# Kernel tuning notes

Measured on AMD Instinct MI355X. Metric: run time of the kernel, lower is better.

Reference implementation:

```python
import jax, jax.numpy as jnp
import numpy as np

N_NODES = 50000


def gcn_conv(x, W, b, src, dst, n):
    """PyG GCNConv: add self-loops, sym-normalize, linear, scatter-add."""
    loop = jnp.arange(n, dtype=src.dtype)
    s = jnp.concatenate([src, loop])  # [E+N]
    d = jnp.concatenate([dst, loop])
    deg = jax.ops.segment_sum(jnp.ones_like(s, dtype=x.dtype), d, num_segments=n)
    dinv = jnp.where(deg > 0, jax.lax.rsqrt(deg), 0.0)  # deg^-1/2
    norm = dinv[s] * dinv[d]  # [E+N]
    h = x @ W  # [N, out] dense GEMM first (in >= out)
    msg = h[s] * norm[:, None]  # gather + scale
    out = jax.ops.segment_sum(msg, d, num_segments=n)  # scatter-add
    return out + b


def setup_inputs() -> dict:
    key = jax.random.key(0)
    k1, k2, k3, k4, k5, k6, k7, k8 = jax.random.split(key, 8)
    in_c, hid_c, out_c = 512, 128, 64
    n, e, l = N_NODES, 800000, 100000
    x = jax.random.normal(k1, (n, in_c), dtype=jnp.float32)
    edge_index = jax.random.randint(k2, (2, e), 0, n, dtype=jnp.int64)
    edge_label_index = jax.random.randint(k3, (2, l), 0, n, dtype=jnp.int64)
    # Glorot-ish init for weights, zeros for biases (PyG default bias=zeros)
    W1 = jax.random.normal(k4, (in_c, hid_c), dtype=jnp.float32) / np.sqrt(in_c)
    b1 = jnp.zeros((hid_c,), dtype=jnp.float32)
    W2 = jax.random.normal(k5, (hid_c, out_c), dtype=jnp.float32) / np.sqrt(hid_c)
    b2 = jnp.zeros((out_c,), dtype=jnp.float32)
    return {"x": x, "edge_index": edge_index, "edge_label_index": edge_label_index,
            "W1": W1, "b1": b1, "W2": W2, "b2": b2}


def reference(x, edge_index, edge_label_index, W1, b1, W2, b2):
    n = x.shape[0]
    src, dst = edge_index[0], edge_index[1]
    z = jax.nn.relu(gcn_conv(x, W1, b1, src, dst, n))
    z = gcn_conv(z, W2, b2, src, dst, n)
    es, ed = edge_label_index[0], edge_label_index[1]
    return jnp.sum(z[es] * z[ed], axis=-1).reshape(-1)
```

## Files before the change

### kernel.cpp

```cpp
#include <hip/hip_runtime.h>

#define IN_C  512
#define HID_C 128
#define OUT_C 64

using short8 = __attribute__((ext_vector_type(8))) short;
using floatx4 = __attribute__((ext_vector_type(4))) float;

__device__ inline unsigned short f2bf(float f) {
    unsigned u = __builtin_bit_cast(unsigned, f);
    u += 0x7FFFu + ((u >> 16) & 1u);
    return (unsigned short)(u >> 16);
}
__device__ inline float bf2f(unsigned short h) {
    unsigned u = ((unsigned)h) << 16;
    return __builtin_bit_cast(float, u);
}

__global__ void k_zero_int(int* __restrict__ p, int n) {
    int i = blockIdx.x * blockDim.x + threadIdx.x;
    if (i < n) p[i] = 0;
}

__global__ void k_count(const int* __restrict__ dst, int* __restrict__ cnt, int e) {
    int i = blockIdx.x * blockDim.x + threadIdx.x;
    if (i < e) atomicAdd(&cnt[dst[i]], 1);
}

__global__ void k_dinv(const int* __restrict__ cnt, float* __restrict__ dinv, int n) {
    int i = blockIdx.x * blockDim.x + threadIdx.x;
    if (i < n) dinv[i] = rsqrtf(1.0f + (float)cnt[i]);
}

__global__ void k_blocksum(const int* __restrict__ cnt, int* __restrict__ bsum, int n) {
    __shared__ int sdata[256];
    int t = threadIdx.x;
    int i = blockIdx.x * 256 + t;
    sdata[t] = (i < n) ? cnt[i] : 0;
    __syncthreads();
    for (int s = 128; s > 0; s >>= 1) {
        if (t < s) sdata[t] += sdata[t + s];
        __syncthreads();
    }
    if (t == 0) bsum[blockIdx.x] = sdata[0];
}

__global__ void k_scanpartials(int* __restrict__ bsum, int nb) {
    __shared__ int sdata[256];
    int t = threadIdx.x;
    int orig = (t < nb) ? bsum[t] : 0;
    sdata[t] = orig;
    __syncthreads();
    for (int off = 1; off < 256; off <<= 1) {
        int v = (t >= off) ? sdata[t - off] : 0;
        __syncthreads();
        sdata[t] += v;
        __syncthreads();
    }
    if (t < nb) bsum[t] = sdata[t] - orig;
}

__global__ void k_scanfinal(const int* __restrict__ cnt, const int* __restrict__ bsum_ex,
                            int* __restrict__ row_ptr, int n, int e_total) {
    __shared__ int sdata[256];
    int t = threadIdx.x;
    int i = blockIdx.x * 256 + t;
    int orig = (i < n) ? cnt[i] : 0;
    sdata[t] = orig;
    __syncthreads();
    for (int off = 1; off < 256; off <<= 1) {
        int v = (t >= off) ? sdata[t - off] : 0;
        __syncthreads();
        sdata[t] += v;
        __syncthreads();
    }
    if (i < n) row_ptr[i] = sdata[t] - orig + bsum_ex[blockIdx.x];
    if (i == 0) row_ptr[n] = e_total;
}

__global__ void k_fill(const int* __restrict__ src, const int* __restrict__ dst,
                       const int* __restrict__ row_ptr, int* __restrict__ cur,
                       int* __restrict__ col, int e) {
    int i = blockIdx.x * blockDim.x + threadIdx.x;
    if (i < e) {
        int d = dst[i];
        int pos = atomicAdd(&cur[d], 1);
        col[row_ptr[d] + pos] = src[i];
    }
}

__global__ void k_prep_w(const float* __restrict__ W, unsigned short* __restrict__ hi,
                         unsigned short* __restrict__ lo, int K, int N) {
    int i = blockIdx.x * blockDim.x + threadIdx.x;
    if (i >= K * N) return;
    int k = i / N, n = i % N;
    float v = W[i];
    unsigned short h = f2bf(v);
    float r = v - bf2f(h);
    hi[(long)n * K + k] = h;
    lo[(long)n * K + k] = f2bf(r);
}

template <int K, int NPW>
__global__ __launch_bounds__(256) void k_gemm_mfma(
    const float* __restrict__ A, const unsigned short* __restrict__ Bt_hi,
    const unsigned short* __restrict__ Bt_lo, const float* __restrict__ dinv,
    float* __restrict__ Hs, int M) {
    constexpr int N = 64 * NPW;
    constexpr int LDA = 72;
    constexpr int NT = K / 64;
    __shared__ __align__(16) unsigned short As_hi[2][64 * LDA];
    __shared__ __align__(16) unsigned short As_lo[2][64 * LDA];

    const int tid = threadIdx.x;
    const int w = tid >> 6;
    const int lane = tid & 63;
    const int m = lane & 15;
    const int quad = lane >> 4;
    const int m0 = blockIdx.x * 64;

    const int srow = tid >> 4;
    const int skk = (tid & 15) << 2;

    floatx4 acc[4][NPW];
#pragma unroll
    for (int mi = 0; mi < 4; ++mi)
#pragma unroll
        for (int ni = 0; ni < NPW; ++ni) acc[mi][ni] = (floatx4){0.f, 0.f, 0.f, 0.f};

    float4 pf[4];
#pragma unroll
    for (int i = 0; i < 4; ++i) {
        int gm = m0 + srow + 16 * i;
        pf[i] = make_float4(0.f, 0.f, 0.f, 0.f);
        if (gm < M) pf[i] = *(const float4*)&A[(long)gm * K + skk];
    }
#pragma unroll
    for (int i = 0; i < 4; ++i) {
        ushort4 h, l;
        h.x = f2bf(pf[i].x); l.x = f2bf(pf[i].x - bf2f(h.x));
        h.y = f2bf(pf[i].y); l.y = f2bf(pf[i].y - bf2f(h.y));
        h.z = f2bf(pf[i].z); l.z = f2bf(pf[i].z - bf2f(h.z));
        h.w = f2bf(pf[i].w); l.w = f2bf(pf[i].w - bf2f(h.w));
        int off = (srow + 16 * i) * LDA + skk;
        *(ushort4*)&As_hi[0][off] = h;
        *(ushort4*)&As_lo[0][off] = l;
    }

    for (int t = 0; t < NT; ++t) {
        __syncthreads();
        const int buf = t & 1;
        if (t + 1 < NT) {
#pragma unroll
            for (int i = 0; i < 4; ++i) {
                int gm = m0 + srow + 16 * i;
                pf[i] = make_float4(0.f, 0.f, 0.f, 0.f);
                if (gm < M) pf[i] = *(const float4*)&A[(long)gm * K + (t + 1) * 64 + skk];
            }
        }
#pragma unroll
        for (int s = 0; s < 2; ++s) {
            short8 ah[4], al[4];
#pragma unroll
            for (int mi = 0; mi < 4; ++mi) {
                int off = (mi * 16 + m) * LDA + s * 32 + quad * 8;
                ah[mi] = *(const short8*)&As_hi[buf][off];
                al[mi] = *(const short8*)&As_lo[buf][off];
            }
#pragma unroll
            for (int ni = 0; ni < NPW; ++ni) {
                int n = (w * NPW + ni) * 16 + m;
                long boff = (long)n * K + t * 64 + s * 32 + quad * 8;
                short8 bh = *(const short8*)&Bt_hi[boff];
                short8 bl = *(const short8*)&Bt_lo[boff];
#pragma unroll
                for (int mi = 0; mi < 4; ++mi) {
                    acc[mi][ni] = __builtin_amdgcn_mfma_f32_16x16x32_bf16(ah[mi], bh, acc[mi][ni], 0, 0, 0);
                    acc[mi][ni] = __builtin_amdgcn_mfma_f32_16x16x32_bf16(ah[mi], bl, acc[mi][ni], 0, 0, 0);
                    acc[mi][ni] = __builtin_amdgcn_mfma_f32_16x16x32_bf16(al[mi], bh, acc[mi][ni], 0, 0, 0);
                }
            }
        }
        if (t + 1 < NT) {
#pragma unroll
            for (int i = 0; i < 4; ++i) {
                ushort4 h, l;
                h.x = f2bf(pf[i].x); l.x = f2bf(pf[i].x - bf2f(h.x));
                h.y = f2bf(pf[i].y); l.y = f2bf(pf[i].y - bf2f(h.y));
                h.z = f2bf(pf[i].z); l.z = f2bf(pf[i].z - bf2f(h.z));
                h.w = f2bf(pf[i].w); l.w = f2bf(pf[i].w - bf2f(h.w));
                int off = (srow + 16 * i) * LDA + skk;
                *(ushort4*)&As_hi[buf ^ 1][off] = h;
                *(ushort4*)&As_lo[buf ^ 1][off] = l;
            }
        }
    }

#pragma unroll
    for (int mi = 0; mi < 4; ++mi) {
#pragma unroll
        for (int r = 0; r < 4; ++r) {
            int row = m0 + mi * 16 + quad * 4 + r;
            if (row < M) {
                float dv = dinv[row];
#pragma unroll
                for (int ni = 0; ni < NPW; ++ni) {
                    int n = (w * NPW + ni) * 16 + m;
                    Hs[(long)row * N + n] = acc[mi][ni][r] * dv;
                }
            }
        }
    }
}

__global__ __launch_bounds__(256) void k_agg1(
    const float* __restrict__ h, const int* __restrict__ row_ptr,
    const int* __restrict__ col, const float* __restrict__ dinv,
    const float* __restrict__ bias, float* __restrict__ z, int n) {
    int node = blockIdx.x * 4 + (threadIdx.x >> 6);
    node = __builtin_amdgcn_readfirstlane(node);
    if (node >= n) return;
    int lane = threadIdx.x & 63;
    const float2* hp = (const float2*)h;
    float2 acc = hp[(long)node * 64 + lane];
    int rs = row_ptr[node], re = row_ptr[node + 1];
    int j = rs;
    for (; j + 4 <= re; j += 4) {
        int s0 = col[j], s1 = col[j + 1], s2 = col[j + 2], s3 = col[j + 3];
        float2 v0 = hp[(long)s0 * 64 + lane];
        float2 v1 = hp[(long)s1 * 64 + lane];
        float2 v2 = hp[(long)s2 * 64 + lane];
        float2 v3 = hp[(long)s3 * 64 + lane];
        acc.x += v0.x + v1.x + v2.x + v3.x;
        acc.y += v0.y + v1.y + v2.y + v3.y;
    }
    for (; j < re; ++j) {
        int s = col[j];
        float2 v = hp[(long)s * 64 + lane];
        acc.x += v.x;
        acc.y += v.y;
    }
    float dv = dinv[node];
    float2 b = ((const float2*)bias)[lane];
    acc.x = fmaxf(fmaf(acc.x, dv, b.x), 0.f);
    acc.y = fmaxf(fmaf(acc.y, dv, b.y), 0.f);
    ((float2*)z)[(long)node * 64 + lane] = acc;
}

__global__ __launch_bounds__(256) void k_agg2(
    const float* __restrict__ h, const int* __restrict__ row_ptr,
    const int* __restrict__ col, const float* __restrict__ dinv,
    const float* __restrict__ bias, float* __restrict__ z, int n) {
    int node = blockIdx.x * 4 + (threadIdx.x >> 6);
    node = __builtin_amdgcn_readfirstlane(node);
    if (node >= n) return;
    int lane = threadIdx.x & 63;
    float acc = h[(long)node * 64 + lane];
    int rs = row_ptr[node], re = row_ptr[node + 1];
    int j = rs;
    for (; j + 4 <= re; j += 4) {
        int s0 = col[j], s1 = col[j + 1], s2 = col[j + 2], s3 = col[j + 3];
        acc += h[(long)s0 * 64 + lane] + h[(long)s1 * 64 + lane] +
               h[(long)s2 * 64 + lane] + h[(long)s3 * 64 + lane];
    }
    for (; j < re; ++j) acc += h[(long)col[j] * 64 + lane];
    z[(long)node * 64 + lane] = fmaf(acc, dinv[node], bias[lane]);
}

__global__ void k_dot(const float* __restrict__ z2, const int* __restrict__ es,
                      const int* __restrict__ ed, float* __restrict__ out, int L) {
    int gid = blockIdx.x * blockDim.x + threadIdx.x;
    int wid = gid >> 6;
    int lane = threadIdx.x & 63;
    if (wid >= L) return;
    int a = es[wid], b = ed[wid];
    float v = z2[(long)a * OUT_C + lane] * z2[(long)b * OUT_C + lane];
#pragma unroll
    for (int off = 32; off > 0; off >>= 1) v += __shfl_down(v, off);
    if (lane == 0) out[wid] = v;
}

extern "C" void kernel_launch(void* const* d_in, const int* in_sizes, int n_in,
                              void* d_out, int out_size, void* d_ws, size_t ws_size,
                              hipStream_t stream) {
    const float* x = (const float*)d_in[0];
    const int* ei = (const int*)d_in[1];
    const int* eli = (const int*)d_in[2];
    const float* W1 = (const float*)d_in[3];
    const float* b1 = (const float*)d_in[4];
    const float* W2 = (const float*)d_in[5];
    const float* b2 = (const float*)d_in[6];
    float* out = (float*)d_out;

    const int N = in_sizes[0] / IN_C;
    const int E = in_sizes[1] / 2;
    const int L = in_sizes[2] / 2;
    const int* src = ei;
    const int* dst = ei + E;
    const int* es = eli;
    const int* ed = eli + L;

    const int Npad = (N + 63) & ~63;
    const int Epad = (E + 3) & ~3;

    int* cnt = (int*)d_ws;
    int* cur = cnt + Npad;
    int* row_ptr = cur + Npad;
    int* bsum = row_ptr + Npad + 64;
    int* col = bsum + 256;
    float* dinv = (float*)(col + Epad);
    float* h1s = dinv + Npad;
    float* z1 = h1s + (long)N * HID_C;
    float* h2s = h1s;
    float* z2 = h1s + (long)N * OUT_C;
    unsigned short* wt1_hi = (unsigned short*)(z1 + (long)N * HID_C);
    unsigned short* wt1_lo = wt1_hi + IN_C * HID_C;
    unsigned short* wt2_hi = wt1_lo + IN_C * HID_C;
    unsigned short* wt2_lo = wt2_hi + HID_C * OUT_C;

    const int TPB = 256;
    const int nb = (N + 255) / 256;

    k_prep_w<<<(IN_C * HID_C + TPB - 1) / TPB, TPB, 0, stream>>>(W1, wt1_hi, wt1_lo, IN_C, HID_C);
    k_prep_w<<<(HID_C * OUT_C + TPB - 1) / TPB, TPB, 0, stream>>>(W2, wt2_hi, wt2_lo, HID_C, OUT_C);

    k_zero_int<<<(2 * Npad + TPB - 1) / TPB, TPB, 0, stream>>>(cnt, 2 * Npad);
    k_count<<<(E + TPB - 1) / TPB, TPB, 0, stream>>>(dst, cnt, E);
    k_dinv<<<(N + TPB - 1) / TPB, TPB, 0, stream>>>(cnt, dinv, N);
    k_blocksum<<<nb, 256, 0, stream>>>(cnt, bsum, N);
    k_scanpartials<<<1, 256, 0, stream>>>(bsum, nb);
    k_scanfinal<<<nb, 256, 0, stream>>>(cnt, bsum, row_ptr, N, E);
    k_fill<<<(E + TPB - 1) / TPB, TPB, 0, stream>>>(src, dst, row_ptr, cur, col, E);

    k_gemm_mfma<IN_C, 2><<<(N + 63) / 64, 256, 0, stream>>>(x, wt1_hi, wt1_lo, dinv, h1s, N);
    k_agg1<<<(N + 3) / 4, 256, 0, stream>>>(h1s, row_ptr, col, dinv, b1, z1, N);

    k_gemm_mfma<HID_C, 1><<<(N + 63) / 64, 256, 0, stream>>>(z1, wt2_hi, wt2_lo, dinv, h2s, N);
    k_agg2<<<(N + 3) / 4, 256, 0, stream>>>(h2s, row_ptr, col, dinv, b2, z2, N);

    k_dot<<<((long)L * 64 + TPB - 1) / TPB, TPB, 0, stream>>>(z2, es, ed, out, L);
}
```

Before: 405.6 us.

## Replace LDS-staged split-bf16 GEMM with per-wave direct-from-global register pipeline

The GEMM kernel stops staging A tiles through shared memory and drops its block barriers. Each wave now loads its own A rows and B columns straight from global memory into registers, using a one-step register prefetch. The hi part of each value is taken by truncation instead of rounding. Each wave handles a 64-row by 32-column tile, so A rows are re-read from global memory by several waves in exchange for removing LDS traffic and syncs.

```diff
diff --git a/kernel.cpp b/kernel.cpp
--- a/kernel.cpp
+++ b/kernel.cpp
@@ -15,6 +15,20 @@
 __device__ inline float bf2f(unsigned short h) {
     unsigned u = ((unsigned)h) << 16;
     return __builtin_bit_cast(float, u);
+}
+
+__device__ inline void split8(const float4& u, const float4& v, short8& hi, short8& lo) {
+    float f[8] = {u.x, u.y, u.z, u.w, v.x, v.y, v.z, v.w};
+    union { unsigned short s[8]; short8 v8; } H, L;
+#pragma unroll
+    for (int j = 0; j < 8; ++j) {
+        unsigned ub = __builtin_bit_cast(unsigned, f[j]);
+        unsigned hb = ub & 0xFFFF0000u;
+        H.s[j] = (unsigned short)(hb >> 16);
+        L.s[j] = f2bf(f[j] - __builtin_bit_cast(float, hb));
+    }
+    hi = H.v8;
+    lo = L.v8;
 }
 
 __global__ void k_zero_int(int* __restrict__ p, int n) {
@@ -101,98 +115,97 @@
     lo[(long)n * K + k] = f2bf(r);
 }
 
-template <int K, int NPW>
-__global__ __launch_bounds__(256) void k_gemm_mfma(
-    const float* __restrict__ A, const unsigned short* __restrict__ Bt_hi,
-    const unsigned short* __restrict__ Bt_lo, const float* __restrict__ dinv,
+template <int K, int N, int NI>
+__global__ __launch_bounds__(256) void k_gemm_direct(
+    const float* __restrict__ A, const unsigned short* __restrict__ Bth,
+    const unsigned short* __restrict__ Btl, const float* __restrict__ dinv,
     float* __restrict__ Hs, int M) {
-    constexpr int N = 64 * NPW;
-    constexpr int LDA = 72;
-    constexpr int NT = K / 64;
-    __shared__ __align__(16) unsigned short As_hi[2][64 * LDA];
-    __shared__ __align__(16) unsigned short As_lo[2][64 * LDA];
-
-    const int tid = threadIdx.x;
-    const int w = tid >> 6;
-    const int lane = tid & 63;
+    constexpr int CS = N / (16 * NI);
+    constexpr int NT = K / 32;
+    const int gw = (blockIdx.x * 256 + threadIdx.x) >> 6;
+    const int lane = threadIdx.x & 63;
+    const int rb = gw / CS;
+    const int cs = gw % CS;
+    const int row0 = rb * 64;
+    if (row0 >= M) return;
     const int m = lane & 15;
     const int quad = lane >> 4;
-    const int m0 = blockIdx.x * 64;
-
-    const int srow = tid >> 4;
-    const int skk = (tid & 15) << 2;
-
-    floatx4 acc[4][NPW];
+
+    bool rowok[4];
+    const float* ap[4];
+#pragma unroll
+    for (int mi = 0; mi < 4; ++mi) {
+        rowok[mi] = (row0 + mi * 16) < M;
+        int r = rowok[mi] ? (row0 + mi * 16 + m) : 0;
+        ap[mi] = A + (long)r * K + quad * 8;
+    }
+    const unsigned short* bhp[NI];
+    const unsigned short* blp[NI];
+#pragma unroll
+    for (int ni = 0; ni < NI; ++ni) {
+        int n = (cs * NI + ni) * 16 + m;
+        bhp[ni] = Bth + (long)n * K + quad * 8;
+        blp[ni] = Btl + (long)n * K + quad * 8;
+    }
+
+    floatx4 acc[4][NI];
 #pragma unroll
     for (int mi = 0; mi < 4; ++mi)
 #pragma unroll
-        for (int ni = 0; ni < NPW; ++ni) acc[mi][ni] = (floatx4){0.f, 0.f, 0.f, 0.f};
-
-    float4 pf[4];
-#pragma unroll
-    for (int i = 0; i < 4; ++i) {
-        int gm = m0 + srow + 16 * i;
-        pf[i] = make_float4(0.f, 0.f, 0.f, 0.f);
-        if (gm < M) pf[i] = *(const float4*)&A[(long)gm * K + skk];
-    }
-#pragma unroll
-    for (int i = 0; i < 4; ++i) {
-        ushort4 h, l;
-        h.x = f2bf(pf[i].x); l.x = f2bf(pf[i].x - bf2f(h.x));
-        h.y = f2bf(pf[i].y); l.y = f2bf(pf[i].y - bf2f(h.y));
-        h.z = f2bf(pf[i].z); l.z = f2bf(pf[i].z - bf2f(h.z));
-        h.w = f2bf(pf[i].w); l.w = f2bf(pf[i].w - bf2f(h.w));
-        int off = (srow + 16 * i) * LDA + skk;
-        *(ushort4*)&As_hi[0][off] = h;
-        *(ushort4*)&As_lo[0][off] = l;
+        for (int ni = 0; ni < NI; ++ni) acc[mi][ni] = (floatx4){0.f, 0.f, 0.f, 0.f};
+
+    float4 cu[4], cv[4], pu[4], pv[4];
+    short8 cbh[NI], cbl[NI], pbh[NI], pbl[NI];
+
+#pragma unroll
+    for (int mi = 0; mi < 4; ++mi) {
+        cu[mi] = make_float4(0.f, 0.f, 0.f, 0.f);
+        cv[mi] = make_float4(0.f, 0.f, 0.f, 0.f);
+        if (rowok[mi]) {
+            cu[mi] = *(const float4*)(ap[mi]);
+            cv[mi] = *(const float4*)(ap[mi] + 4);
+        }
+    }
+#pragma unroll
+    for (int ni = 0; ni < NI; ++ni) {
+        cbh[ni] = *(const short8*)(bhp[ni]);
+        cbl[ni] = *(const short8*)(blp[ni]);
     }
 
     for (int t = 0; t < NT; ++t) {
-        __syncthreads();
-        const int buf = t & 1;
         if (t + 1 < NT) {
 #pragma unroll
-            for (int i = 0; i < 4; ++i) {
-                int gm = m0 + srow + 16 * i;
-                pf[i] = make_float4(0.f, 0.f, 0.f, 0.f);
-                if (gm < M) pf[i] = *(const float4*)&A[(long)gm * K + (t + 1) * 64 + skk];
-            }
-        }
-#pragma unroll
-        for (int s = 0; s < 2; ++s) {
-            short8 ah[4], al[4];
-#pragma unroll
             for (int mi = 0; mi < 4; ++mi) {
-                int off = (mi * 16 + m) * LDA + s * 32 + quad * 8;
-                ah[mi] = *(const short8*)&As_hi[buf][off];
-                al[mi] = *(const short8*)&As_lo[buf][off];
-            }
-#pragma unroll
-            for (int ni = 0; ni < NPW; ++ni) {
-                int n = (w * NPW + ni) * 16 + m;
-                long boff = (long)n * K + t * 64 + s * 32 + quad * 8;
-                short8 bh = *(const short8*)&Bt_hi[boff];
-                short8 bl = *(const short8*)&Bt_lo[boff];
-#pragma unroll
-                for (int mi = 0; mi < 4; ++mi) {
-                    acc[mi][ni] = __builtin_amdgcn_mfma_f32_16x16x32_bf16(ah[mi], bh, acc[mi][ni], 0, 0, 0);
-                    acc[mi][ni] = __builtin_amdgcn_mfma_f32_16x16x32_bf16(ah[mi], bl, acc[mi][ni], 0, 0, 0);
-                    acc[mi][ni] = __builtin_amdgcn_mfma_f32_16x16x32_bf16(al[mi], bh, acc[mi][ni], 0, 0, 0);
+                pu[mi] = make_float4(0.f, 0.f, 0.f, 0.f);
+                pv[mi] = make_float4(0.f, 0.f, 0.f, 0.f);
+                if (rowok[mi]) {
+                    pu[mi] = *(const float4*)(ap[mi] + (t + 1) * 32);
+                    pv[mi] = *(const float4*)(ap[mi] + (t + 1) * 32 + 4);
                 }
             }
+#pragma unroll
+            for (int ni = 0; ni < NI; ++ni) {
+                pbh[ni] = *(const short8*)(bhp[ni] + (t + 1) * 32);
+                pbl[ni] = *(const short8*)(blp[ni] + (t + 1) * 32);
+            }
+        }
+        short8 ah[4], al[4];
+#pragma unroll
+        for (int mi = 0; mi < 4; ++mi) split8(cu[mi], cv[mi], ah[mi], al[mi]);
+#pragma unroll
+        for (int ni = 0; ni < NI; ++ni) {
+#pragma unroll
+            for (int mi = 0; mi < 4; ++mi) {
+                acc[mi][ni] = __builtin_amdgcn_mfma_f32_16x16x32_bf16(ah[mi], cbh[ni], acc[mi][ni], 0, 0, 0);
+                acc[mi][ni] = __builtin_amdgcn_mfma_f32_16x16x32_bf16(ah[mi], cbl[ni], acc[mi][ni], 0, 0, 0);
+                acc[mi][ni] = __builtin_amdgcn_mfma_f32_16x16x32_bf16(al[mi], cbh[ni], acc[mi][ni], 0, 0, 0);
+            }
         }
         if (t + 1 < NT) {
 #pragma unroll
-            for (int i = 0; i < 4; ++i) {
-                ushort4 h, l;
-                h.x = f2bf(pf[i].x); l.x = f2bf(pf[i].x - bf2f(h.x));
-                h.y = f2bf(pf[i].y); l.y = f2bf(pf[i].y - bf2f(h.y));
-                h.z = f2bf(pf[i].z); l.z = f2bf(pf[i].z - bf2f(h.z));
-                h.w = f2bf(pf[i].w); l.w = f2bf(pf[i].w - bf2f(h.w));
-                int off = (srow + 16 * i) * LDA + skk;
-                *(ushort4*)&As_hi[buf ^ 1][off] = h;
-                *(ushort4*)&As_lo[buf ^ 1][off] = l;
-            }
+            for (int mi = 0; mi < 4; ++mi) { cu[mi] = pu[mi]; cv[mi] = pv[mi]; }
+#pragma unroll
+            for (int ni = 0; ni < NI; ++ni) { cbh[ni] = pbh[ni]; cbl[ni] = pbl[ni]; }
         }
     }
 
@@ -200,12 +213,12 @@
     for (int mi = 0; mi < 4; ++mi) {
 #pragma unroll
         for (int r = 0; r < 4; ++r) {
-            int row = m0 + mi * 16 + quad * 4 + r;
+            int row = row0 + mi * 16 + quad * 4 + r;
             if (row < M) {
                 float dv = dinv[row];
 #pragma unroll
-                for (int ni = 0; ni < NPW; ++ni) {
-                    int n = (w * NPW + ni) * 16 + m;
+                for (int ni = 0; ni < NI; ++ni) {
+                    int n = (cs * NI + ni) * 16 + m;
                     Hs[(long)row * N + n] = acc[mi][ni][r] * dv;
                 }
             }
@@ -332,10 +345,18 @@
     k_scanfinal<<<nb, 256, 0, stream>>>(cnt, bsum, row_ptr, N, E);
     k_fill<<<(E + TPB - 1) / TPB, TPB, 0, stream>>>(src, dst, row_ptr, cur, col, E);
 
-    k_gemm_mfma<IN_C, 2><<<(N + 63) / 64, 256, 0, stream>>>(x, wt1_hi, wt1_lo, dinv, h1s, N);
+    {
+        int waves = ((N + 63) / 64) * (HID_C / 32);
+        k_gemm_direct<IN_C, HID_C, 2>
+            <<<(waves + 3) / 4, 256, 0, stream>>>(x, wt1_hi, wt1_lo, dinv, h1s, N);
+    }
     k_agg1<<<(N + 3) / 4, 256, 0, stream>>>(h1s, row_ptr, col, dinv, b1, z1, N);
 
-    k_gemm_mfma<HID_C, 1><<<(N + 63) / 64, 256, 0, stream>>>(z1, wt2_hi, wt2_lo, dinv, h2s, N);
+    {
+        int waves = ((N + 63) / 64) * (OUT_C / 32);
+        k_gemm_direct<HID_C, OUT_C, 2>
+            <<<(waves + 3) / 4, 256, 0, stream>>>(z1, wt2_hi, wt2_lo, dinv, h2s, N);
+    }
     k_agg2<<<(N + 3) / 4, 256, 0, stream>>>(h2s, row_ptr, col, dinv, b2, z2, N);
 
     k_dot<<<((long)L * 64 + TPB - 1) / TPB, TPB, 0, stream>>>(z2, es, ed, out, L);
```

Measured after the change: 442.5 us. +9.1%, slower.

## Stage weight tiles in shared memory and use 2x2 warp tiling in GEMM

Applied to the files above, without the earlier changes.

Rewrites the dense GEMM kernel so that each k-tile of the pre-split bf16 weights is staged in LDS alongside the A tile. The four warps are arranged as a 2x2 grid over M and N instead of each warp covering all rows. The hi/lo split of A now truncates to get the hi part and rounds only the residual, and the padding changes to 68. This replaces the per-warp global reads of B that were repeated in every block with shared-memory reuse, and gives each warp a more balanced tile. In exchange, the A/B double buffer becomes a single buffer with two barriers per k step. The truncated hi part also slightly changes the rounding of the split.

```diff
diff --git a/kernel.cpp b/kernel.cpp
--- a/kernel.cpp
+++ b/kernel.cpp
@@ -15,6 +15,21 @@
 __device__ inline float bf2f(unsigned short h) {
     unsigned u = ((unsigned)h) << 16;
     return __builtin_bit_cast(float, u);
+}
+
+__device__ inline void split_f4(const float4 v, uint2& hp, uint2& lp) {
+    unsigned u0 = __builtin_bit_cast(unsigned, v.x);
+    unsigned u1 = __builtin_bit_cast(unsigned, v.y);
+    unsigned u2 = __builtin_bit_cast(unsigned, v.z);
+    unsigned u3 = __builtin_bit_cast(unsigned, v.w);
+    hp.x = (u1 & 0xFFFF0000u) | (u0 >> 16);
+    hp.y = (u3 & 0xFFFF0000u) | (u2 >> 16);
+    float r0 = v.x - __builtin_bit_cast(float, u0 & 0xFFFF0000u);
+    float r1 = v.y - __builtin_bit_cast(float, u1 & 0xFFFF0000u);
+    float r2 = v.z - __builtin_bit_cast(float, u2 & 0xFFFF0000u);
+    float r3 = v.w - __builtin_bit_cast(float, u3 & 0xFFFF0000u);
+    lp.x = ((unsigned)f2bf(r0)) | (((unsigned)f2bf(r1)) << 16);
+    lp.y = ((unsigned)f2bf(r2)) | (((unsigned)f2bf(r3)) << 16);
 }
 
 __global__ void k_zero_int(int* __restrict__ p, int n) {
@@ -101,112 +116,131 @@
     lo[(long)n * K + k] = f2bf(r);
 }
 
-template <int K, int NPW>
-__global__ __launch_bounds__(256) void k_gemm_mfma(
-    const float* __restrict__ A, const unsigned short* __restrict__ Bt_hi,
-    const unsigned short* __restrict__ Bt_lo, const float* __restrict__ dinv,
+template <int K, int BN>
+__global__ __launch_bounds__(256) void k_gemm_tile(
+    const float* __restrict__ A, const unsigned short* __restrict__ Bth,
+    const unsigned short* __restrict__ Btl, const float* __restrict__ dinv,
     float* __restrict__ Hs, int M) {
-    constexpr int N = 64 * NPW;
-    constexpr int LDA = 72;
+    constexpr int NIW = BN / 32;
+    constexpr int MI = 2;
     constexpr int NT = K / 64;
-    __shared__ __align__(16) unsigned short As_hi[2][64 * LDA];
-    __shared__ __align__(16) unsigned short As_lo[2][64 * LDA];
+    constexpr int LP = 68;
+    __shared__ __align__(16) unsigned short Ah[64 * LP];
+    __shared__ __align__(16) unsigned short Al[64 * LP];
+    __shared__ __align__(16) unsigned short Bh[BN * LP];
+    __shared__ __align__(16) unsigned short Bl[BN * LP];
 
     const int tid = threadIdx.x;
-    const int w = tid >> 6;
-    const int lane = tid & 63;
-    const int m = lane & 15;
-    const int quad = lane >> 4;
+    const int w = tid >> 6, lane = tid & 63;
+    const int wr = w >> 1, wc = w & 1;
+    const int m = lane & 15, quad = lane >> 4;
     const int m0 = blockIdx.x * 64;
 
-    const int srow = tid >> 4;
-    const int skk = (tid & 15) << 2;
-
-    floatx4 acc[4][NPW];
-#pragma unroll
-    for (int mi = 0; mi < 4; ++mi)
-#pragma unroll
-        for (int ni = 0; ni < NPW; ++ni) acc[mi][ni] = (floatx4){0.f, 0.f, 0.f, 0.f};
-
-    float4 pf[4];
+    const int sr = tid & 63;
+    const int sq = tid >> 6;
+    int gm = m0 + sr;
+    if (gm >= M) gm = M - 1;
+    const float* ga = A + (long)gm * K + sq * 16;
+
+    const int sb = tid >> 1;
+    const int hb = tid & 1;
+    const bool bok = sb < BN;
+    const unsigned short* gbh = Bth + (long)(bok ? sb : 0) * K + hb * 32;
+    const unsigned short* gbl = Btl + (long)(bok ? sb : 0) * K + hb * 32;
+
+    floatx4 acc[MI][NIW];
+#pragma unroll
+    for (int mi = 0; mi < MI; ++mi)
+#pragma unroll
+        for (int ni = 0; ni < NIW; ++ni) acc[mi][ni] = (floatx4){0.f, 0.f, 0.f, 0.f};
+
+    float4 va[4];
+    uint4 vbh[4], vbl[4];
+
+#pragma unroll
+    for (int i = 0; i < 4; ++i) va[i] = *(const float4*)(ga + i * 4);
 #pragma unroll
     for (int i = 0; i < 4; ++i) {
-        int gm = m0 + srow + 16 * i;
-        pf[i] = make_float4(0.f, 0.f, 0.f, 0.f);
-        if (gm < M) pf[i] = *(const float4*)&A[(long)gm * K + skk];
-    }
-#pragma unroll
-    for (int i = 0; i < 4; ++i) {
-        ushort4 h, l;
-        h.x = f2bf(pf[i].x); l.x = f2bf(pf[i].x - bf2f(h.x));
-        h.y = f2bf(pf[i].y); l.y = f2bf(pf[i].y - bf2f(h.y));
-        h.z = f2bf(pf[i].z); l.z = f2bf(pf[i].z - bf2f(h.z));
-        h.w = f2bf(pf[i].w); l.w = f2bf(pf[i].w - bf2f(h.w));
-        int off = (srow + 16 * i) * LDA + skk;
-        *(ushort4*)&As_hi[0][off] = h;
-        *(ushort4*)&As_lo[0][off] = l;
+        vbh[i] = *(const uint4*)(gbh + i * 8);
+        vbl[i] = *(const uint4*)(gbl + i * 8);
     }
 
     for (int t = 0; t < NT; ++t) {
         __syncthreads();
-        const int buf = t & 1;
+        {
+            uint4 hq[2], lq[2];
+#pragma unroll
+            for (int j = 0; j < 2; ++j) {
+                uint2 h0, l0, h1, l1;
+                split_f4(va[2 * j + 0], h0, l0);
+                split_f4(va[2 * j + 1], h1, l1);
+                hq[j].x = h0.x; hq[j].y = h0.y; hq[j].z = h1.x; hq[j].w = h1.y;
+                lq[j].x = l0.x; lq[j].y = l0.y; lq[j].z = l1.x; lq[j].w = l1.y;
+            }
+            const int base = sr * LP + sq * 16;
+            *(uint4*)&Ah[base + 0] = hq[0];
+            *(uint4*)&Ah[base + 8] = hq[1];
+            *(uint4*)&Al[base + 0] = lq[0];
+            *(uint4*)&Al[base + 8] = lq[1];
+            if (bok) {
+                const int bb = sb * LP + hb * 32;
+#pragma unroll
+                for (int i = 0; i < 4; ++i) *(uint4*)&Bh[bb + 8 * i] = vbh[i];
+#pragma unroll
+                for (int i = 0; i < 4; ++i) *(uint4*)&Bl[bb + 8 * i] = vbl[i];
+            }
+        }
+        __syncthreads();
+
         if (t + 1 < NT) {
+            const int k0 = (t + 1) * 64;
+#pragma unroll
+            for (int i = 0; i < 4; ++i) va[i] = *(const float4*)(ga + k0 + i * 4);
 #pragma unroll
             for (int i = 0; i < 4; ++i) {
-                int gm = m0 + srow + 16 * i;
-                pf[i] = make_float4(0.f, 0.f, 0.f, 0.f);
-                if (gm < M) pf[i] = *(const float4*)&A[(long)gm * K + (t + 1) * 64 + skk];
+                vbh[i] = *(const uint4*)(gbh + k0 + i * 8);
+                vbl[i] = *(const uint4*)(gbl + k0 + i * 8);
             }
         }
+
 #pragma unroll
         for (int s = 0; s < 2; ++s) {
-            short8 ah[4], al[4];
-#pragma unroll
-            for (int mi = 0; mi < 4; ++mi) {
-                int off = (mi * 16 + m) * LDA + s * 32 + quad * 8;
-                ah[mi] = *(const short8*)&As_hi[buf][off];
-                al[mi] = *(const short8*)&As_lo[buf][off];
-            }
-#pragma unroll
-            for (int ni = 0; ni < NPW; ++ni) {
-                int n = (w * NPW + ni) * 16 + m;
-                long boff = (long)n * K + t * 64 + s * 32 + quad * 8;
-                short8 bh = *(const short8*)&Bt_hi[boff];
-                short8 bl = *(const short8*)&Bt_lo[boff];
-#pragma unroll
-                for (int mi = 0; mi < 4; ++mi) {
-                    acc[mi][ni] = __builtin_amdgcn_mfma_f32_16x16x32_bf16(ah[mi], bh, acc[mi][ni], 0, 0, 0);
-                    acc[mi][ni] = __builtin_amdgcn_mfma_f32_16x16x32_bf16(ah[mi], bl, acc[mi][ni], 0, 0, 0);
-                    acc[mi][ni] = __builtin_amdgcn_mfma_f32_16x16x32_bf16(al[mi], bh, acc[mi][ni], 0, 0, 0);
+            short8 ah[MI], al[MI];
+#pragma unroll
+            for (int mi = 0; mi < MI; ++mi) {
+                const int off = (wr * 32 + mi * 16 + m) * LP + s * 32 + quad * 8;
+                ah[mi] = *(const short8*)&Ah[off];
+                al[mi] = *(const short8*)&Al[off];
+            }
+            short8 bh[NIW], bl[NIW];
+#pragma unroll
+            for (int ni = 0; ni < NIW; ++ni) {
+                const int off = (wc * (BN / 2) + ni * 16 + m) * LP + s * 32 + quad * 8;
+                bh[ni] = *(const short8*)&Bh[off];
+                bl[ni] = *(const short8*)&Bl[off];
+            }
+#pragma unroll
+            for (int ni = 0; ni < NIW; ++ni)
+#pragma unroll
+                for (int mi = 0; mi < MI; ++mi) {
+                    acc[mi][ni] = __builtin_amdgcn_mfma_f32_16x16x32_bf16(ah[mi], bh[ni], acc[mi][ni], 0, 0, 0);
+                    acc[mi][ni] = __builtin_amdgcn_mfma_f32_16x16x32_bf16(ah[mi], bl[ni], acc[mi][ni], 0, 0, 0);
+                    acc[mi][ni] = __builtin_amdgcn_mfma_f32_16x16x32_bf16(al[mi], bh[ni], acc[mi][ni], 0, 0, 0);
                 }
-            }
         }
-        if (t + 1 < NT) {
-#pragma unroll
-            for (int i = 0; i < 4; ++i) {
-                ushort4 h, l;
-                h.x = f2bf(pf[i].x); l.x = f2bf(pf[i].x - bf2f(h.x));
-                h.y = f2bf(pf[i].y); l.y = f2bf(pf[i].y - bf2f(h.y));
-                h.z = f2bf(pf[i].z); l.z = f2bf(pf[i].z - bf2f(h.z));
-                h.w = f2bf(pf[i].w); l.w = f2bf(pf[i].w - bf2f(h.w));
-                int off = (srow + 16 * i) * LDA + skk;
-                *(ushort4*)&As_hi[buf ^ 1][off] = h;
-                *(ushort4*)&As_lo[buf ^ 1][off] = l;
-            }
-        }
-    }
-
-#pragma unroll
-    for (int mi = 0; mi < 4; ++mi) {
+    }
+
+#pragma unroll
+    for (int mi = 0; mi < MI; ++mi) {
 #pragma unroll
         for (int r = 0; r < 4; ++r) {
-            int row = m0 + mi * 16 + quad * 4 + r;
+            const int row = m0 + wr * 32 + mi * 16 + quad * 4 + r;
             if (row < M) {
-                float dv = dinv[row];
-#pragma unroll
-                for (int ni = 0; ni < NPW; ++ni) {
-                    int n = (w * NPW + ni) * 16 + m;
-                    Hs[(long)row * N + n] = acc[mi][ni][r] * dv;
+                const float dv = dinv[row];
+#pragma unroll
+                for (int ni = 0; ni < NIW; ++ni) {
+                    const int n = wc * (BN / 2) + ni * 16 + m;
+                    Hs[(long)row * BN + n] = acc[mi][ni][r] * dv;
                 }
             }
         }
@@ -332,10 +366,12 @@
     k_scanfinal<<<nb, 256, 0, stream>>>(cnt, bsum, row_ptr, N, E);
     k_fill<<<(E + TPB - 1) / TPB, TPB, 0, stream>>>(src, dst, row_ptr, cur, col, E);
 
-    k_gemm_mfma<IN_C, 2><<<(N + 63) / 64, 256, 0, stream>>>(x, wt1_hi, wt1_lo, dinv, h1s, N);
+    k_gemm_tile<IN_C, HID_C>
+        <<<(N + 63) / 64, 256, 0, stream>>>(x, wt1_hi, wt1_lo, dinv, h1s, N);
     k_agg1<<<(N + 3) / 4, 256, 0, stream>>>(h1s, row_ptr, col, dinv, b1, z1, N);
 
-    k_gemm_mfma<HID_C, 1><<<(N + 63) / 64, 256, 0, stream>>>(z1, wt2_hi, wt2_lo, dinv, h2s, N);
+    k_gemm_tile<HID_C, OUT_C>
+        <<<(N + 63) / 64, 256, 0, stream>>>(z1, wt2_hi, wt2_lo, dinv, h2s, N);
     k_agg2<<<(N + 3) / 4, 256, 0, stream>>>(h2s, row_ptr, col, dinv, b2, z2, N);
 
     k_dot<<<((long)L * 64 + TPB - 1) / TPB, TPB, 0, stream>>>(z2, es, ed, out, L);
```

Measured after the change: 472.6 us. +16.5%, slower.
